# Optimization experiments

Hardware: AMD Instinct MI355X
Metric: run time of the kernel (lower is better)

The kernel has to match this reference:

```python
import jax, jax.numpy as jnp
import numpy as np

H = 512   # hidden_dim
D = 512   # token feature dim (GRU input_size)
A = 256   # attn_dim
V = 10000 # vocab_size
TE = 256  # encoder timesteps
TD = 128  # decoder timesteps


def setup_inputs() -> dict:
    key = jax.random.key(0)
    ks = jax.random.split(key, 18)
    f = lambda k, shape, s: jax.random.normal(k, shape, jnp.float32) * s
    return {
        "x": f(ks[0], (1, TE, D), 1.0),
        "y": f(ks[1], (1, TD, D), 1.0),
        # encoder GRU params (PyTorch layout: gates [r|z|n] stacked)
        "Wi_e": f(ks[2], (3 * H, D), 0.04), "Wh_e": f(ks[3], (3 * H, H), 0.04),
        "bi_e": f(ks[4], (3 * H,), 0.04), "bh_e": f(ks[5], (3 * H,), 0.04),
        # decoder GRU params
        "Wi_d": f(ks[6], (3 * H, D), 0.04), "Wh_d": f(ks[7], (3 * H, H), 0.04),
        "bi_d": f(ks[8], (3 * H,), 0.04), "bh_d": f(ks[9], (3 * H,), 0.04),
        # additive attention params
        "Wh_attn": f(ks[10], (A, H), 0.06), "Ws_attn": f(ks[11], (A, H), 0.06),
        "b_attn": f(ks[12], (A,), 0.06), "v_attn": f(ks[13], (A,), 0.06),
        # output projections
        "W1": f(ks[14], (2 * V, 2 * H), 0.03), "b1": f(ks[15], (2 * V,), 0.03),
        "W2": f(ks[16], (V, 2 * V), 0.02), "b2": f(ks[17], (V,), 0.02),
    }


def _gru_gates(gi, gh, h):
    # gi/gh: [..., 3H] stacked input/hidden gate pre-activations, h: [..., H]
    ir, iz, inn = jnp.split(gi, 3, axis=-1)
    hr, hz, hn = jnp.split(gh, 3, axis=-1)
    r = jax.nn.sigmoid(ir + hr)
    z = jax.nn.sigmoid(iz + hz)
    n = jnp.tanh(inn + r * hn)
    return (1.0 - z) * n + z * h


def reference(x, y, Wi_e, Wh_e, bi_e, bh_e, Wi_d, Wh_d, bi_d, bh_d,
              Wh_attn, Ws_attn, b_attn, v_attn, W1, b1, W2, b2):
    X = x[0]  # [TE, D]
    Y = y[0]  # [TD, D]

    # Encoder: original calls self.encoder per single token with NO carried
    # hidden state, so each h_i is one GRU step from zero hidden. Vectorized:
    gi = X @ Wi_e.T + bi_e                      # [TE, 3H]
    gh = jnp.broadcast_to(bh_e, gi.shape)       # zero hidden -> only bias
    enc_H = _gru_gates(gi, gh, jnp.zeros((X.shape[0], H), X.dtype))  # [TE, H]
    h0 = enc_H[-1]                              # encoder_hidden_last

    # Decoder GRU over y with initial hidden h0
    def step(h, x_t):
        gi_t = x_t @ Wi_d.T + bi_d
        gh_t = h @ Wh_d.T + bh_d
        h_new = _gru_gates(gi_t, gh_t, h)
        return h_new, h_new

    _, dec_S = jax.lax.scan(step, h0, Y)        # [TD, H]

    # Bahdanau additive attention, fully batched over (TD, TE)
    encP = enc_H @ Wh_attn.T                    # [TE, A]
    decP = dec_S @ Ws_attn.T                    # [TD, A]
    e = jnp.tanh(encP[None, :, :] + decP[:, None, :] + b_attn)  # [TD, TE, A]
    scores = jnp.einsum('tea,a->te', e, v_attn)  # [TD, TE]
    attn = jax.nn.softmax(scores, axis=1)        # softmax over encoder steps
    context = attn @ enc_H                       # [TD, H]

    concat = jnp.concatenate([context, dec_S], axis=-1)  # [TD, 2H]
    out = concat @ W1.T + b1                     # [TD, 2V]
    out = out @ W2.T + b2                        # [TD, V]
    return out
```

## Files before the change

kernel.cpp:

```cpp
#include <hip/hip_runtime.h>
#include <stdint.h>

#define HID 512
#define THREE_H 1536
#define ADIM 256
#define NVOC 10000
#define TEnc 256
#define TDec 128

typedef float f32x4 __attribute__((ext_vector_type(4)));
typedef __bf16 bf16x8 __attribute__((ext_vector_type(8)));

__device__ __forceinline__ unsigned short f2bf(float f) {
  union { float f; unsigned u; } v; v.f = f;
  unsigned r = v.u + 0x7FFFu + ((v.u >> 16) & 1u);
  return (unsigned short)(r >> 16);
}
__device__ __forceinline__ float sigmoidf_(float x) { return 1.f / (1.f + __expf(-x)); }
__device__ __forceinline__ float tanh_fast(float x) {
  float ax = fabsf(x);
  float e = __expf(ax + ax);
  float t = 1.f - 2.f / (e + 1.f);
  return copysignf(t, x);
}

__device__ __forceinline__ void st_u64_sys(unsigned long long* p, unsigned long long v) {
  asm volatile("global_store_dwordx2 %0, %1, off sc0 sc1" :: "v"(p), "v"(v) : "memory");
}
__device__ __forceinline__ unsigned long long ld_u64_sys(const unsigned long long* p) {
  unsigned long long a;
  asm volatile("global_load_dwordx2 %0, %1, off sc0 sc1\n\ts_waitcnt vmcnt(0)"
               : "=&v"(a) : "v"(p) : "memory");
  return a;
}

#define GLDS16(gp, lp)                                                                 \
  __builtin_amdgcn_global_load_lds((const __attribute__((address_space(1))) void*)(gp),\
                                   (__attribute__((address_space(3))) void*)(lp), 16, 0, 0)

__global__ void cvt_xy(const float* __restrict__ x, const float* __restrict__ y,
                       unsigned short* __restrict__ xb, unsigned short* __restrict__ yb) {
  int i = (blockIdx.x * blockDim.x + threadIdx.x) * 4;
  const float* src;
  unsigned short* dst;
  int j;
  if (i < TEnc * HID) { src = x; dst = xb; j = i; }
  else { src = y; dst = yb; j = i - TEnc * HID; }
  float4 v = *(const float4*)(src + j);
  ushort4 o;
  o.x = f2bf(v.x); o.y = f2bf(v.y); o.z = f2bf(v.z); o.w = f2bf(v.w);
  *(ushort4*)(dst + j) = o;
}

template <int BN, int BK>
__global__ __launch_bounds__(256, 1) void gemm_bt(
    const unsigned short* __restrict__ Abf, const float* __restrict__ B,
    const float* __restrict__ bias, float* __restrict__ C, unsigned short* __restrict__ Cbf,
    int M, int N, int K) {
  constexpr int NF = BN / 16;
  constexpr int B4 = BN * BK / 1024;
  constexpr int AG = BK / 16;
  constexpr int KK = BK / 32;
  extern __shared__ char smem[];
  unsigned short* Al0 = (unsigned short*)smem;
  unsigned short* Al1 = Al0 + 128 * BK;
  unsigned short* Bl0 = Al1 + 128 * BK;
  unsigned short* Bl1 = Bl0 + BN * BK;

  const int tid = threadIdx.x;
  const int lane = tid & 63;
  const int wid = tid >> 6;
  const int m0 = blockIdx.x * 128;
  const int n0 = blockIdx.y * BN;
  const int NT = K / BK;

  float4 breg[B4];
  f32x4 acc[2][NF];
#pragma unroll
  for (int i = 0; i < 2; ++i)
#pragma unroll
    for (int j = 0; j < NF; ++j) acc[i][j] = (f32x4){0.f, 0.f, 0.f, 0.f};

  auto stageA = [&](int t, unsigned short* dst) {
    const unsigned short* Ab = Abf + (size_t)m0 * K + (size_t)t * BK;
#pragma unroll
    for (int g = 0; g < AG; ++g) {
      int elem = g * 2048 + tid * 8;
      int arow = elem / BK;
      int acol = elem - arow * BK;
      GLDS16(Ab + (size_t)arow * K + acol, (char*)dst + g * 4096 + wid * 1024);
    }
  };
  auto loadB = [&](int t) {
    const float* Bb = B + (size_t)t * BK;
#pragma unroll
    for (int p = 0; p < B4; ++p) {
      int e = (p * 256 + tid) * 4;
      int brow = e / BK;
      int bcol = e - brow * BK;
      int grow = n0 + brow;
      if (grow > N - 1) grow = N - 1;
      breg[p] = *(const float4*)(Bb + (size_t)grow * K + bcol);
    }
  };
  auto writeB = [&](unsigned short* dst) {
#pragma unroll
    for (int p = 0; p < B4; ++p) {
      ushort4 o;
      o.x = f2bf(breg[p].x); o.y = f2bf(breg[p].y);
      o.z = f2bf(breg[p].z); o.w = f2bf(breg[p].w);
      *(ushort4*)((char*)dst + (p * 256 + tid) * 8) = o;
    }
  };

  stageA(0, Al0);
  loadB(0);
  for (int t = 0; t < NT; ++t) {
    unsigned short* Ac = (t & 1) ? Al1 : Al0;
    unsigned short* Bc = (t & 1) ? Bl1 : Bl0;
    asm volatile("s_waitcnt vmcnt(0)" ::: "memory");
    writeB(Bc);
    __syncthreads();
    if (t + 1 < NT) {
      stageA(t + 1, (t & 1) ? Al0 : Al1);
      loadB(t + 1);
    }
    const int r0 = lane & 15;
    const int kb = (lane >> 4) * 8;
#pragma unroll
    for (int kk = 0; kk < KK; ++kk) {
      int ko = kk * 32 + kb;
      bf16x8 a0 = *(const bf16x8*)(Ac + (wid * 32 + r0) * BK + ko);
      bf16x8 a1 = *(const bf16x8*)(Ac + (wid * 32 + 16 + r0) * BK + ko);
#pragma unroll
      for (int nf = 0; nf < NF; ++nf) {
        bf16x8 bb = *(const bf16x8*)(Bc + (nf * 16 + r0) * BK + ko);
        acc[0][nf] = __builtin_amdgcn_mfma_f32_16x16x32_bf16(a0, bb, acc[0][nf], 0, 0, 0);
        acc[1][nf] = __builtin_amdgcn_mfma_f32_16x16x32_bf16(a1, bb, acc[1][nf], 0, 0, 0);
      }
    }
  }
  const int cc = lane & 15;
  const int rq = (lane >> 4) * 4;
#pragma unroll
  for (int mi = 0; mi < 2; ++mi) {
    int row = m0 + wid * 32 + mi * 16 + rq;
#pragma unroll
    for (int nf = 0; nf < NF; ++nf) {
      int col = n0 + nf * 16 + cc;
      if (col < N) {
        float bv = bias ? bias[col] : 0.f;
#pragma unroll
        for (int j = 0; j < 4; ++j) {
          float v = acc[mi][nf][j] + bv;
          if (C) C[(size_t)(row + j) * N + col] = v;
          if (Cbf) Cbf[(size_t)(row + j) * N + col] = f2bf(v);
        }
      }
    }
  }
}

__global__ __launch_bounds__(256, 1) void gemm_enc(
    const unsigned short* __restrict__ Abf, const float* __restrict__ Wi,
    const float* __restrict__ bi, const float* __restrict__ bh,
    float* __restrict__ encH, unsigned short* __restrict__ encHbf) {
  constexpr int BN = 96, BK = 128, NF = 6, B4 = 12, AG = 8, KK = 4, K = 512;
  extern __shared__ char smem[];
  unsigned short* Al0 = (unsigned short*)smem;
  unsigned short* Al1 = Al0 + 128 * BK;
  unsigned short* Bl0 = Al1 + 128 * BK;
  unsigned short* Bl1 = Bl0 + BN * BK;

  const int tid = threadIdx.x;
  const int lane = tid & 63;
  const int wid = tid >> 6;
  const int m0 = blockIdx.x * 128;
  const int n0g = blockIdx.y * 32;
  const int NT = K / BK;

  float4 breg[B4];
  f32x4 acc[2][NF];
#pragma unroll
  for (int i = 0; i < 2; ++i)
#pragma unroll
    for (int j = 0; j < NF; ++j) acc[i][j] = (f32x4){0.f, 0.f, 0.f, 0.f};

  auto stageA = [&](int t, unsigned short* dst) {
    const unsigned short* Ab = Abf + (size_t)m0 * K + (size_t)t * BK;
#pragma unroll
    for (int g = 0; g < AG; ++g) {
      int elem = g * 2048 + tid * 8;
      int arow = elem >> 7;
      int acol = elem & 127;
      GLDS16(Ab + (size_t)arow * K + acol, (char*)dst + g * 4096 + wid * 1024);
    }
  };
  auto loadB = [&](int t) {
    const float* Bb = Wi + (size_t)t * BK;
#pragma unroll
    for (int p = 0; p < B4; ++p) {
      int e = (p * 256 + tid) * 4;
      int brow = e >> 7;
      int bcol = e & 127;
      int grow = (brow >> 5) * HID + n0g + (brow & 31);
      breg[p] = *(const float4*)(Bb + (size_t)grow * K + bcol);
    }
  };
  auto writeB = [&](unsigned short* dst) {
#pragma unroll
    for (int p = 0; p < B4; ++p) {
      ushort4 o;
      o.x = f2bf(breg[p].x); o.y = f2bf(breg[p].y);
      o.z = f2bf(breg[p].z); o.w = f2bf(breg[p].w);
      *(ushort4*)((char*)dst + (p * 256 + tid) * 8) = o;
    }
  };

  stageA(0, Al0);
  loadB(0);
  for (int t = 0; t < NT; ++t) {
    unsigned short* Ac = (t & 1) ? Al1 : Al0;
    unsigned short* Bc = (t & 1) ? Bl1 : Bl0;
    asm volatile("s_waitcnt vmcnt(0)" ::: "memory");
    writeB(Bc);
    __syncthreads();
    if (t + 1 < NT) {
      stageA(t + 1, (t & 1) ? Al0 : Al1);
      loadB(t + 1);
    }
    const int r0 = lane & 15;
    const int kb = (lane >> 4) * 8;
#pragma unroll
    for (int kk = 0; kk < KK; ++kk) {
      int ko = kk * 32 + kb;
      bf16x8 a0 = *(const bf16x8*)(Ac + (wid * 32 + r0) * BK + ko);
      bf16x8 a1 = *(const bf16x8*)(Ac + (wid * 32 + 16 + r0) * BK + ko);
#pragma unroll
      for (int nf = 0; nf < NF; ++nf) {
        bf16x8 bb = *(const bf16x8*)(Bc + (nf * 16 + r0) * BK + ko);
        acc[0][nf] = __builtin_amdgcn_mfma_f32_16x16x32_bf16(a0, bb, acc[0][nf], 0, 0, 0);
        acc[1][nf] = __builtin_amdgcn_mfma_f32_16x16x32_bf16(a1, bb, acc[1][nf], 0, 0, 0);
      }
    }
  }
  const int cc = lane & 15;
  const int rq = (lane >> 4) * 4;
#pragma unroll
  for (int mi = 0; mi < 2; ++mi) {
    int row = m0 + wid * 32 + mi * 16 + rq;
#pragma unroll
    for (int nfj = 0; nfj < 2; ++nfj) {
      int j = n0g + nfj * 16 + cc;
      float br_ = bi[j] + bh[j];
      float bz_ = bi[HID + j] + bh[HID + j];
      float bin_ = bi[2 * HID + j];
      float bhn_ = bh[2 * HID + j];
#pragma unroll
      for (int jj = 0; jj < 4; ++jj) {
        float r = sigmoidf_(acc[mi][nfj][jj] + br_);
        float z = sigmoidf_(acc[mi][nfj + 2][jj] + bz_);
        float n = tanh_fast(acc[mi][nfj + 4][jj] + bin_ + r * bhn_);
        float h = (1.f - z) * n;
        encH[(size_t)(row + jj) * HID + j] = h;
        encHbf[(size_t)(row + jj) * HID + j] = f2bf(h);
      }
    }
  }
}

__global__ __launch_bounds__(256, 1) void gru_scan(
    const float* __restrict__ Whd, const float* __restrict__ bhd,
    const float* __restrict__ giY, const float* __restrict__ h0,
    unsigned long long* __restrict__ hx,
    unsigned short* __restrict__ decSbf, unsigned short* __restrict__ concatbf) {
  __shared__ float hl[548];
  __shared__ float dots[48];
  const int tid = threadIdx.x;
  const int lane = tid & 63, wid = tid >> 6;
  const int g = blockIdx.x;

  const int row16 = lane & 15;
  const int q = lane >> 4;
  float4 wreg[32];
  {
    int wrow = (wid < 3) ? wid : 0;
    const float* wr = Whd + ((size_t)wrow * HID + (size_t)g * 16 + row16) * HID + q * 128;
#pragma unroll
    for (int i = 0; i < 32; ++i) wreg[i] = *(const float4*)(wr + i * 4);
  }
  float bhr = 0.f, bhz = 0.f, bhn = 0.f, hreg = 0.f;
  if (wid == 3 && lane < 16) {
    int jj = g * 16 + lane;
    bhr = bhd[jj]; bhz = bhd[HID + jj]; bhn = bhd[2 * HID + jj];
    hreg = h0[jj];
  }
  {
    int w0 = tid * 2, w1 = tid * 2 + 1;
    hl[w0 + ((w0 >> 7) << 2)] = h0[w0];
    hl[w1 + ((w1 >> 7) << 2)] = h0[w1];
  }
  __syncthreads();

  for (int t = 0; t < TDec; ++t) {
    float gir = 0.f, giz = 0.f, gin = 0.f;
    if (wid < 3) {
      const float4* hp = (const float4*)hl;
      const int hb = q * 33;
      float p0 = 0.f, p1 = 0.f, p2 = 0.f, p3 = 0.f;
#pragma unroll
      for (int i = 0; i < 32; i += 4) {
        float4 ha = hp[hb + i], hv = hp[hb + i + 1], hc = hp[hb + i + 2], hd = hp[hb + i + 3];
        float4 wa = wreg[i], wb = wreg[i + 1], wc = wreg[i + 2], wd = wreg[i + 3];
        p0 += wa.x * ha.x + wa.y * ha.y + wa.z * ha.z + wa.w * ha.w;
        p1 += wb.x * hv.x + wb.y * hv.y + wb.z * hv.z + wb.w * hv.w;
        p2 += wc.x * hc.x + wc.y * hc.y + wc.z * hc.z + wc.w * hc.w;
        p3 += wd.x * hd.x + wd.y * hd.y + wd.z * hd.z + wd.w * hd.w;
      }
      float p = (p0 + p1) + (p2 + p3);
      p += __shfl_xor(p, 16);
      p += __shfl_xor(p, 32);
      if (lane < 16) dots[wid * 16 + lane] = p;
    } else if (lane < 16) {
      int jj = g * 16 + lane;
      const float* gi = giY + (size_t)t * THREE_H;
      gir = gi[jj]; giz = gi[HID + jj]; gin = gi[2 * HID + jj];
    }
    __syncthreads();
    unsigned long long* hxB = hx + (size_t)(t & 1) * 256 * 16;
    if (wid == 3 && lane < 16) {
      int jj = g * 16 + lane;
      float r = sigmoidf_(gir + dots[lane] + bhr);
      float z = sigmoidf_(giz + dots[16 + lane] + bhz);
      float n = tanh_fast(gin + r * (dots[32 + lane] + bhn));
      float hn = (1.f - z) * n + z * hreg;
      hreg = hn;
      unsigned short hb16 = f2bf(hn);
      unsigned short hb_up = (unsigned short)__shfl_xor((int)hb16, 1);
      if ((lane & 1) == 0) {
        unsigned long long w = ((unsigned long long)(unsigned)(t + 1) << 32) |
                               ((unsigned)hb_up << 16) | (unsigned)hb16;
        st_u64_sys(hxB + (size_t)(g * 8 + (lane >> 1)) * 16, w);
      }
      decSbf[(size_t)t * HID + jj] = hb16;
      concatbf[(size_t)t * 2 * HID + HID + jj] = hb16;
    }
    if (t == TDec - 1) break;
    {
      const unsigned long long* p0 = hxB + (size_t)tid * 16;
      const unsigned tag = (unsigned)(t + 1);
      unsigned long long v;
      int guard = 0;
      do { v = ld_u64_sys(p0); } while ((unsigned)(v >> 32) != tag && ++guard < (1 << 20));
      int w0 = tid * 2, w1 = tid * 2 + 1;
      hl[w0 + ((w0 >> 7) << 2)] = __uint_as_float(((unsigned)v & 0xFFFFu) << 16);
      hl[w1 + ((w1 >> 7) << 2)] = __uint_as_float((((unsigned)v >> 16) & 0xFFFFu) << 16);
    }
    __syncthreads();
  }
}

__global__ __launch_bounds__(256) void attn_ctx(const float* __restrict__ encP,
                                                const float* __restrict__ decP,
                                                const float* __restrict__ vattn,
                                                const float* __restrict__ encH,
                                                unsigned short* __restrict__ concatbf) {
  __shared__ float dp[ADIM], vv[ADIM], pl[TEnc];
  __shared__ float red[8];
  const int t = blockIdx.x, tid = threadIdx.x;
  if (tid < 64) {
    *(float4*)(dp + tid * 4) = *(const float4*)(decP + (size_t)t * ADIM + tid * 4);
    *(float4*)(vv + tid * 4) = *(const float4*)(vattn + tid * 4);
  }
  __syncthreads();
  float s = 0.f;
  const float* ep = encP + (size_t)tid * ADIM;
#pragma unroll 4
  for (int a = 0; a < ADIM; a += 4) {
    float4 e4 = *(const float4*)(ep + a);
    s += vv[a] * tanh_fast(e4.x + dp[a]);
    s += vv[a + 1] * tanh_fast(e4.y + dp[a + 1]);
    s += vv[a + 2] * tanh_fast(e4.z + dp[a + 2]);
    s += vv[a + 3] * tanh_fast(e4.w + dp[a + 3]);
  }
  float m = s;
#pragma unroll
  for (int off = 32; off; off >>= 1) m = fmaxf(m, __shfl_xor(m, off));
  if ((tid & 63) == 0) red[tid >> 6] = m;
  __syncthreads();
  m = fmaxf(fmaxf(red[0], red[1]), fmaxf(red[2], red[3]));
  float p = __expf(s - m);
  pl[tid] = p;
  float sum = p;
#pragma unroll
  for (int off = 32; off; off >>= 1) sum += __shfl_xor(sum, off);
  if ((tid & 63) == 0) red[4 + (tid >> 6)] = sum;
  __syncthreads();
  float inv = 1.f / (red[4] + red[5] + red[6] + red[7]);
  float a0 = 0.f, a1 = 0.f;
  for (int e = 0; e < TEnc; ++e) {
    float pe = pl[e];
    a0 += pe * encH[(size_t)e * HID + tid];
    a1 += pe * encH[(size_t)e * HID + tid + 256];
  }
  concatbf[(size_t)t * 2 * HID + tid] = f2bf(a0 * inv);
  concatbf[(size_t)t * 2 * HID + tid + 256] = f2bf(a1 * inv);
}

extern "C" void kernel_launch(void* const* d_in, const int* in_sizes, int n_in,
                              void* d_out, int out_size, void* d_ws, size_t ws_size,
                              hipStream_t stream) {
  const float* x = (const float*)d_in[0];
  const float* y = (const float*)d_in[1];
  const float* Wi_e = (const float*)d_in[2];
  const float* bi_e = (const float*)d_in[4];
  const float* bh_e = (const float*)d_in[5];
  const float* Wi_d = (const float*)d_in[6];
  const float* Wh_d = (const float*)d_in[7];
  const float* bi_d = (const float*)d_in[8];
  const float* bh_d = (const float*)d_in[9];
  const float* Wh_attn = (const float*)d_in[10];
  const float* Ws_attn = (const float*)d_in[11];
  const float* b_attn = (const float*)d_in[12];
  const float* v_attn = (const float*)d_in[13];
  const float* W1 = (const float*)d_in[14];
  const float* b1 = (const float*)d_in[15];
  const float* W2 = (const float*)d_in[16];
  const float* b2 = (const float*)d_in[17];
  float* out = (float*)d_out;

  char* ws = (char*)d_ws;
  size_t off = 0;
  auto alloc = [&](size_t bytes) {
    char* p = ws + off;
    off += (bytes + 255) & ~(size_t)255;
    return p;
  };
  char* ctrl = alloc(2 * 256 * 128);
  unsigned long long* hx = (unsigned long long*)ctrl;
  unsigned short* Xbf = (unsigned short*)alloc((size_t)TEnc * HID * 2);
  unsigned short* Ybf = (unsigned short*)alloc((size_t)TDec * HID * 2);
  float* giY = (float*)alloc((size_t)TDec * THREE_H * 4);
  float* encH = (float*)alloc((size_t)TEnc * HID * 4);
  unsigned short* encHbf = (unsigned short*)alloc((size_t)TEnc * HID * 2);
  float* encP = (float*)alloc((size_t)TEnc * ADIM * 4);
  float* decP = (float*)alloc((size_t)TDec * ADIM * 4);
  unsigned short* decSbf = (unsigned short*)alloc((size_t)TDec * HID * 2);
  unsigned short* concatbf = (unsigned short*)alloc((size_t)TDec * 2 * HID * 2);
  unsigned short* out1bf = (unsigned short*)alloc((size_t)TDec * 20000 * 2);

  hipMemsetAsync(ctrl, 0, 2 * 256 * 128, stream);

  auto* g32 = gemm_bt<32, 128>;
  auto* g80 = gemm_bt<80, 128>;
  auto* g64 = gemm_bt<64, 160>;
  const int smem32 = (128 + 32) * 128 * 2 * 2;
  const int smem80 = (128 + 80) * 128 * 2 * 2;
  const int smem64 = (128 + 64) * 160 * 2 * 2;
  const int smemEnc = (128 + 96) * 128 * 2 * 2;
  hipFuncSetAttribute((const void*)g32, hipFuncAttributeMaxDynamicSharedMemorySize, smem32);
  hipFuncSetAttribute((const void*)g80, hipFuncAttributeMaxDynamicSharedMemorySize, smem80);
  hipFuncSetAttribute((const void*)g64, hipFuncAttributeMaxDynamicSharedMemorySize, smem64);
  hipFuncSetAttribute((const void*)gemm_enc, hipFuncAttributeMaxDynamicSharedMemorySize, smemEnc);

  cvt_xy<<<(TEnc + TDec) * HID / 1024, 256, 0, stream>>>(x, y, Xbf, Ybf);
  gemm_enc<<<dim3(2, 16), 256, smemEnc, stream>>>(Xbf, Wi_e, bi_e, bh_e, encH, encHbf);
  g32<<<dim3(2, 8), 256, smem32, stream>>>(encHbf, Wh_attn, nullptr, encP, nullptr, 256, 256, 512);
  g32<<<dim3(1, 48), 256, smem32, stream>>>(Ybf, Wi_d, bi_d, giY, nullptr, 128, 1536, 512);
  gru_scan<<<32, 256, 0, stream>>>(Wh_d, bh_d, giY, encH + 255 * HID, hx, decSbf, concatbf);
  g32<<<dim3(1, 8), 256, smem32, stream>>>(decSbf, Ws_attn, b_attn, decP, nullptr, 128, 256, 512);
  attn_ctx<<<TDec, 256, 0, stream>>>(encP, decP, v_attn, encH, concatbf);
  g80<<<dim3(1, 250), 256, smem80, stream>>>(concatbf, W1, b1, nullptr, out1bf, 128, 20000, 1024);
  g64<<<dim3(1, 157), 256, smem64, stream>>>(out1bf, W2, b2, out, nullptr, 128, NVOC, 20000);
}
```

Measured before the change: 637.4 us.

## Confine GRU scan blocks to a single XCD and exchange hidden state via L2 atomics

The decoder GRU scan now launches 256 oversized-LDS blocks and uses the hardware XCD id register plus atomic counters to elect one XCD whose first 32 blocks do the work, while the rest exit. With every participating block on one XCD, per-step hidden-state exchange uses L2-scoped atomic swap/or on padded per-element slots instead of system-scope loads, aiming to cut inter-block synchronisation latency on each of the 128 steps. A system-scope fallback path is kept in case the L2 poll times out. It depends on undocumented scheduling behaviour and on the large shared memory request forcing one block per CU, and it adds extra launch and election overhead.

```diff
diff --git a/kernel.cpp b/kernel.cpp
--- a/kernel.cpp
+++ b/kernel.cpp
@@ -27,11 +27,31 @@
 __device__ __forceinline__ void st_u64_sys(unsigned long long* p, unsigned long long v) {
   asm volatile("global_store_dwordx2 %0, %1, off sc0 sc1" :: "v"(p), "v"(v) : "memory");
 }
-__device__ __forceinline__ unsigned long long ld_u64_sys(const unsigned long long* p) {
-  unsigned long long a;
-  asm volatile("global_load_dwordx2 %0, %1, off sc0 sc1\n\ts_waitcnt vmcnt(0)"
-               : "=&v"(a) : "v"(p) : "memory");
-  return a;
+__device__ __forceinline__ void ld2_u64_sys(const unsigned long long* p0,
+                                            const unsigned long long* p1,
+                                            unsigned long long& a, unsigned long long& b) {
+  asm volatile("global_load_dwordx2 %0, %2, off sc0 sc1\n\t"
+               "global_load_dwordx2 %1, %3, off sc0 sc1\n\t"
+               "s_waitcnt vmcnt(0)"
+               : "=&v"(a), "=&v"(b)
+               : "v"(p0), "v"(p1)
+               : "memory");
+}
+__device__ __forceinline__ void at_swap_l2(unsigned* p, unsigned v) {
+  asm volatile("global_atomic_swap %0, %1, off" :: "v"(p), "v"(v) : "memory");
+}
+__device__ __forceinline__ void at_or4_l2(const unsigned* p0, const unsigned* p1,
+                                          const unsigned* p2, const unsigned* p3,
+                                          unsigned& a, unsigned& b, unsigned& c, unsigned& d) {
+  unsigned z = 0;
+  asm volatile("global_atomic_or %0, %4, %8, off sc0\n\t"
+               "global_atomic_or %1, %5, %8, off sc0\n\t"
+               "global_atomic_or %2, %6, %8, off sc0\n\t"
+               "global_atomic_or %3, %7, %8, off sc0\n\t"
+               "s_waitcnt vmcnt(0)"
+               : "=&v"(a), "=&v"(b), "=&v"(c), "=&v"(d)
+               : "v"(p0), "v"(p1), "v"(p2), "v"(p3), "v"(z)
+               : "memory");
 }
 
 #define GLDS16(gp, lp)                                                                 \
@@ -269,16 +289,38 @@
   }
 }
 
-__global__ __launch_bounds__(256, 1) void gru_scan(
+__global__ __launch_bounds__(256, 1) void gru_scan_xcd(
     const float* __restrict__ Whd, const float* __restrict__ bhd,
     const float* __restrict__ giY, const float* __restrict__ h0,
-    unsigned long long* __restrict__ hx,
+    unsigned* __restrict__ hxA, unsigned long long* __restrict__ hxS,
+    unsigned* __restrict__ cnt, unsigned* __restrict__ winner,
     unsigned short* __restrict__ decSbf, unsigned short* __restrict__ concatbf) {
-  __shared__ float hl[548];
-  __shared__ float dots[48];
+  extern __shared__ char smem[];
+  float* hl = (float*)smem;
+  float* dots = hl + 548;
+  volatile int* slot_sh = (volatile int*)(dots + 48);
   const int tid = threadIdx.x;
   const int lane = tid & 63, wid = tid >> 6;
-  const int g = blockIdx.x;
+
+  if (tid == 0) {
+    unsigned xcd;
+    asm volatile("s_getreg_b32 %0, hwreg(20, 0, 32)" : "=s"(xcd));
+    xcd &= 7u;
+    unsigned slot = atomicAdd(&cnt[xcd], 1u);
+    if (slot == 31u) atomicCAS(winner, 0u, xcd + 1u);
+    unsigned win = 0;
+    if (slot < 32u) {
+      int spin = 0;
+      while ((win = __hip_atomic_load(winner, __ATOMIC_RELAXED,
+                                      __HIP_MEMORY_SCOPE_AGENT)) == 0u &&
+             ++spin < (1 << 20))
+        __builtin_amdgcn_s_sleep(2);
+    }
+    *slot_sh = (slot < 32u && win == xcd + 1u) ? (int)slot : -1;
+  }
+  __syncthreads();
+  const int g = *slot_sh;
+  if (g < 0) return;
 
   const int row16 = lane & 15;
   const int q = lane >> 4;
@@ -327,7 +369,9 @@
       gir = gi[jj]; giz = gi[HID + jj]; gin = gi[2 * HID + jj];
     }
     __syncthreads();
-    unsigned long long* hxB = hx + (size_t)(t & 1) * 256 * 16;
+    const unsigned tagv = (unsigned)(t + 1);
+    unsigned* hxAB = hxA + (size_t)(t & 1) * 512 * 32;
+    unsigned long long* hxSB = hxS + (size_t)(t & 1) * 256;
     if (wid == 3 && lane < 16) {
       int jj = g * 16 + lane;
       float r = sigmoidf_(gir + dots[lane] + bhr);
@@ -336,25 +380,55 @@
       float hn = (1.f - z) * n + z * hreg;
       hreg = hn;
       unsigned short hb16 = f2bf(hn);
+      at_swap_l2(hxAB + (unsigned)jj * 32, (tagv << 16) | (unsigned)hb16);
       unsigned short hb_up = (unsigned short)__shfl_xor((int)hb16, 1);
       if ((lane & 1) == 0) {
-        unsigned long long w = ((unsigned long long)(unsigned)(t + 1) << 32) |
+        unsigned long long w = ((unsigned long long)tagv << 32) |
                                ((unsigned)hb_up << 16) | (unsigned)hb16;
-        st_u64_sys(hxB + (size_t)(g * 8 + (lane >> 1)) * 16, w);
+        st_u64_sys(hxSB + g * 8 + (lane >> 1), w);
       }
       decSbf[(size_t)t * HID + jj] = hb16;
       concatbf[(size_t)t * 2 * HID + HID + jj] = hb16;
     }
     if (t == TDec - 1) break;
-    {
-      const unsigned long long* p0 = hxB + (size_t)tid * 16;
-      const unsigned tag = (unsigned)(t + 1);
-      unsigned long long v;
-      int guard = 0;
-      do { v = ld_u64_sys(p0); } while ((unsigned)(v >> 32) != tag && ++guard < (1 << 20));
-      int w0 = tid * 2, w1 = tid * 2 + 1;
-      hl[w0 + ((w0 >> 7) << 2)] = __uint_as_float(((unsigned)v & 0xFFFFu) << 16);
-      hl[w1 + ((w1 >> 7) << 2)] = __uint_as_float((((unsigned)v >> 16) & 0xFFFFu) << 16);
+    if (tid < 128) {
+      const unsigned* a0 = hxAB + (tid * 4 + 0) * 32;
+      const unsigned* a1 = hxAB + (tid * 4 + 1) * 32;
+      const unsigned* a2 = hxAB + (tid * 4 + 2) * 32;
+      const unsigned* a3 = hxAB + (tid * 4 + 3) * 32;
+      unsigned rr0 = 0, rr1 = 0, rr2 = 0, rr3 = 0, have = 0;
+      __builtin_amdgcn_s_sleep(1);
+      for (int rd = 0; rd < 8 && have != 0xFu; ++rd) {
+        unsigned v0, v1, v2, v3;
+        at_or4_l2(a0, a1, a2, a3, v0, v1, v2, v3);
+        if (!(have & 1u) && (v0 >> 16) == tagv) { rr0 = v0 & 0xFFFFu; have |= 1u; }
+        if (!(have & 2u) && (v1 >> 16) == tagv) { rr1 = v1 & 0xFFFFu; have |= 2u; }
+        if (!(have & 4u) && (v2 >> 16) == tagv) { rr2 = v2 & 0xFFFFu; have |= 4u; }
+        if (!(have & 8u) && (v3 >> 16) == tagv) { rr3 = v3 & 0xFFFFu; have |= 8u; }
+        if (have != 0xFu) __builtin_amdgcn_s_sleep(1);
+      }
+      if (have != 0xFu) {
+        const unsigned long long* s0 = hxSB + tid * 2;
+        const unsigned long long* s1 = s0 + 1;
+        unsigned long long w0 = 0, w1 = 0;
+        bool k0 = false, k1 = false;
+        int gd = 0;
+        while ((!k0 || !k1) && ++gd < (1 << 20)) {
+          unsigned long long xv, yv;
+          ld2_u64_sys(s0, s1, xv, yv);
+          if ((unsigned)(xv >> 32) == tagv) { w0 = xv; k0 = true; }
+          if ((unsigned)(yv >> 32) == tagv) { w1 = yv; k1 = true; }
+        }
+        rr0 = (unsigned)w0 & 0xFFFFu;
+        rr1 = ((unsigned)w0 >> 16) & 0xFFFFu;
+        rr2 = (unsigned)w1 & 0xFFFFu;
+        rr3 = ((unsigned)w1 >> 16) & 0xFFFFu;
+      }
+      int d0 = tid * 4, d1 = d0 + 1, d2 = d0 + 2, d3 = d0 + 3;
+      hl[d0 + ((d0 >> 7) << 2)] = __uint_as_float(rr0 << 16);
+      hl[d1 + ((d1 >> 7) << 2)] = __uint_as_float(rr1 << 16);
+      hl[d2 + ((d2 >> 7) << 2)] = __uint_as_float(rr2 << 16);
+      hl[d3 + ((d3 >> 7) << 2)] = __uint_as_float(rr3 << 16);
     }
     __syncthreads();
   }
@@ -436,8 +510,13 @@
     off += (bytes + 255) & ~(size_t)255;
     return p;
   };
-  char* ctrl = alloc(2 * 256 * 128);
-  unsigned long long* hx = (unsigned long long*)ctrl;
+  const size_t hxA_bytes = 2 * 512 * 128;
+  const size_t hxS_bytes = 2 * 256 * 8;
+  char* ctrl = alloc(hxA_bytes + hxS_bytes + 256);
+  unsigned* hxA = (unsigned*)ctrl;
+  unsigned long long* hxS = (unsigned long long*)(ctrl + hxA_bytes);
+  unsigned* cnt = (unsigned*)(ctrl + hxA_bytes + hxS_bytes);
+  unsigned* winner = cnt + 16;
   unsigned short* Xbf = (unsigned short*)alloc((size_t)TEnc * HID * 2);
   unsigned short* Ybf = (unsigned short*)alloc((size_t)TDec * HID * 2);
   float* giY = (float*)alloc((size_t)TDec * THREE_H * 4);
@@ -449,7 +528,7 @@
   unsigned short* concatbf = (unsigned short*)alloc((size_t)TDec * 2 * HID * 2);
   unsigned short* out1bf = (unsigned short*)alloc((size_t)TDec * 20000 * 2);
 
-  hipMemsetAsync(ctrl, 0, 2 * 256 * 128, stream);
+  hipMemsetAsync(ctrl, 0, hxA_bytes + hxS_bytes + 256, stream);
 
   auto* g32 = gemm_bt<32, 128>;
   auto* g80 = gemm_bt<80, 128>;
@@ -458,16 +537,19 @@
   const int smem80 = (128 + 80) * 128 * 2 * 2;
   const int smem64 = (128 + 64) * 160 * 2 * 2;
   const int smemEnc = (128 + 96) * 128 * 2 * 2;
+  const int smemScan = 100608;
   hipFuncSetAttribute((const void*)g32, hipFuncAttributeMaxDynamicSharedMemorySize, smem32);
   hipFuncSetAttribute((const void*)g80, hipFuncAttributeMaxDynamicSharedMemorySize, smem80);
   hipFuncSetAttribute((const void*)g64, hipFuncAttributeMaxDynamicSharedMemorySize, smem64);
   hipFuncSetAttribute((const void*)gemm_enc, hipFuncAttributeMaxDynamicSharedMemorySize, smemEnc);
+  hipFuncSetAttribute((const void*)gru_scan_xcd, hipFuncAttributeMaxDynamicSharedMemorySize, smemScan);
 
   cvt_xy<<<(TEnc + TDec) * HID / 1024, 256, 0, stream>>>(x, y, Xbf, Ybf);
   gemm_enc<<<dim3(2, 16), 256, smemEnc, stream>>>(Xbf, Wi_e, bi_e, bh_e, encH, encHbf);
   g32<<<dim3(2, 8), 256, smem32, stream>>>(encHbf, Wh_attn, nullptr, encP, nullptr, 256, 256, 512);
   g32<<<dim3(1, 48), 256, smem32, stream>>>(Ybf, Wi_d, bi_d, giY, nullptr, 128, 1536, 512);
-  gru_scan<<<32, 256, 0, stream>>>(Wh_d, bh_d, giY, encH + 255 * HID, hx, decSbf, concatbf);
+  gru_scan_xcd<<<256, 256, smemScan, stream>>>(Wh_d, bh_d, giY, encH + 255 * HID,
+                                               hxA, hxS, cnt, winner, decSbf, concatbf);
   g32<<<dim3(1, 8), 256, smem32, stream>>>(decSbf, Ws_attn, b_attn, decP, nullptr, 128, 256, 512);
   attn_ctx<<<TDec, 256, 0, stream>>>(encP, decP, v_attn, encH, concatbf);
   g80<<<dim3(1, 250), 256, smem80, stream>>>(concatbf, W1, b1, nullptr, out1bf, 128, 20000, 1024);
```

Result: slower. 806.0 us (+26.5%).
